# Optimization experiments

Measured on AMD Instinct MI355X. Metric: run time of the kernel, lower is better.

## Reference

```python
import jax, jax.numpy as jnp
import numpy as np

B, N, IN, OUT, H, F = 4, 2048, 128, 64, 4, 64


def setup_inputs() -> dict:
    key = jax.random.key(0)
    ks = jax.random.split(key, 10)
    h = jax.random.normal(ks[0], (B, N, IN), dtype=jnp.float32)
    projection_matrix = jax.random.uniform(ks[1], (B, N, N), dtype=jnp.float32)
    similarity_matrix = jnp.tanh(jax.random.normal(ks[2], (B, N, N), dtype=jnp.float32))
    quadrant_matrix = jax.random.randint(ks[3], (B, N, N, 2), 0, 4)
    # learned params (xavier-ish scaling); stored as (in, out) so x @ W
    W = jax.random.normal(ks[4], (IN, OUT * H), dtype=jnp.float32) * (1.0 / np.sqrt(IN))
    random_projection = jax.random.normal(ks[5], (IN, F), dtype=jnp.float32) * 0.1
    a_q = jax.random.normal(ks[6], (2 * F, OUT), dtype=jnp.float32) * (1.0 / np.sqrt(2 * F))
    a_k = jax.random.normal(ks[7], (2 * F, OUT), dtype=jnp.float32) * (1.0 / np.sqrt(2 * F))
    quadrant_bias = jax.random.normal(ks[8], (4, 4), dtype=jnp.float32) * 0.02
    output_proj = jax.random.normal(ks[9], (OUT * H, OUT), dtype=jnp.float32) * (1.0 / np.sqrt(OUT * H))
    return {
        "h": h,
        "projection_matrix": projection_matrix,
        "similarity_matrix": similarity_matrix,
        "W": W,
        "random_projection": random_projection,
        "a_q": a_q,
        "a_k": a_k,
        "quadrant_bias": quadrant_bias,
        "output_proj": output_proj,
        "quadrant_matrix": quadrant_matrix,
    }


def reference(h, projection_matrix, similarity_matrix, W, random_projection,
              a_q, a_k, quadrant_bias, output_proj, quadrant_matrix):
    # random feature map: phi = [cos(h R), sin(h R)]  -> (B, N, 2F)
    proj = jnp.einsum('bnd,df->bnf', h, random_projection)
    phi = jnp.concatenate([jnp.cos(proj), jnp.sin(proj)], axis=-1)
    Q = phi @ a_q                       # (B, N, OUT)
    K = phi @ a_k                       # (B, N, OUT)
    Wh = (h @ W).reshape(h.shape[0], h.shape[1], H, OUT)  # (B, N, H, OUT)

    scores = jnp.einsum('bio,bjo->bij', Q, K)             # (B, N, N)
    # additive relational biases (shared across heads)
    qb = quadrant_bias[quadrant_matrix[..., 0], quadrant_matrix[..., 1]]  # (B, N, N)
    scores = scores + projection_matrix + similarity_matrix + qb
    attn = jax.nn.softmax(scores[:, None, :, :], axis=-1)  # (B, H, N, N) via broadcast

    # aggregate values per head, then concat heads
    hp = jnp.einsum('bhij,bjhk->bihk', attn, Wh)           # (B, N, H, OUT)
    hp = hp.reshape(h.shape[0], h.shape[1], H * OUT)
    out = hp @ output_proj                                  # (B, N, OUT)
    return jax.nn.elu(out)
```

## Files before the change

### kernel.cpp

```cpp
#include <hip/hip_runtime.h>
#include <math.h>

#define BB   4
#define NN   2048
#define IND  128
#define CDIM 256
#define NIT  16

typedef _Float16 half_t;
typedef _Float16 half4_t __attribute__((ext_vector_type(4)));
typedef _Float16 half8_t __attribute__((ext_vector_type(8)));
typedef float    f32x4   __attribute__((ext_vector_type(4)));

#define SHIFT 16.0f

__global__ __launch_bounds__(256) void precompute_kernel(
    const float* __restrict__ hg,
    const float* __restrict__ W,
    const float* __restrict__ R,
    const float* __restrict__ aq,
    const float* __restrict__ ak,
    half_t* __restrict__ Qw,
    half_t* __restrict__ Kw,
    half_t* __restrict__ WhJ)
{
    const int tid  = threadIdx.x;
    const int row0 = blockIdx.x * 16;

    __shared__ float hs[16][IND];
    __shared__ float phis[16][IND];

    {
        const float4* src = (const float4*)(hg + (size_t)row0 * IND);
        float4* dst = (float4*)&hs[0][0];
        dst[tid]       = src[tid];
        dst[tid + 256] = src[tid + 256];
    }
    __syncthreads();

    {
        const int f  = tid & 63;
        const int rr = tid >> 6;
        float p0 = 0.f, p1 = 0.f, p2 = 0.f, p3 = 0.f;
        #pragma unroll 8
        for (int d = 0; d < IND; ++d) {
            const float rv = R[d * 64 + f];
            p0 += hs[rr][d] * rv;      p1 += hs[rr + 4][d] * rv;
            p2 += hs[rr + 8][d] * rv;  p3 += hs[rr + 12][d] * rv;
        }
        float s, c;
        __sincosf(p0, &s, &c); phis[rr][f]      = c; phis[rr][f + 64]      = s;
        __sincosf(p1, &s, &c); phis[rr + 4][f]  = c; phis[rr + 4][f + 64]  = s;
        __sincosf(p2, &s, &c); phis[rr + 8][f]  = c; phis[rr + 8][f + 64]  = s;
        __sincosf(p3, &s, &c); phis[rr + 12][f] = c; phis[rr + 12][f + 64] = s;
    }

    {
        float acc[16];
        #pragma unroll
        for (int r = 0; r < 16; ++r) acc[r] = 0.f;
        #pragma unroll 4
        for (int d = 0; d < IND; ++d) {
            const float w = W[d * CDIM + tid];
            #pragma unroll
            for (int r = 0; r < 16; ++r) acc[r] += hs[r][d] * w;
        }
        const int b   = row0 >> 11;
        const int j16 = (row0 & (NN - 1)) >> 4;
        half8_t v0, v1;
        #pragma unroll
        for (int r = 0; r < 8; ++r) { v0[r] = (half_t)acc[r]; v1[r] = (half_t)acc[r + 8]; }
        half8_t* dst = (half8_t*)(WhJ + (((size_t)b * 128 + j16) * CDIM + tid) * 16);
        dst[0] = v0; dst[1] = v1;
    }
    __syncthreads();

    {
        const int o  = tid & 63;
        const int qk = (tid >> 6) & 1;
        const int rh = tid >> 7;
        const float* A = qk ? ak : aq;
        half_t*    Dst = qk ? Kw : Qw;
        float acc[8];
        #pragma unroll
        for (int r = 0; r < 8; ++r) acc[r] = 0.f;
        #pragma unroll 4
        for (int tt = 0; tt < IND; ++tt) {
            const float a = A[tt * 64 + o];
            #pragma unroll
            for (int r = 0; r < 8; ++r) acc[r] += phis[rh * 8 + r][tt] * a;
        }
        #pragma unroll
        for (int r = 0; r < 8; ++r)
            Dst[(size_t)(row0 + rh * 8 + r) * 64 + o] = (half_t)acc[r];
    }
}

__global__ __launch_bounds__(512, 4) void attn3_kernel(
    const half_t* __restrict__ Qw, const half_t* __restrict__ Kw,
    const half_t* __restrict__ WhJ,
    const float* __restrict__ pm,
    const float* __restrict__ sm,
    const int*   __restrict__ qm,
    const float* __restrict__ qbias,
    const float* __restrict__ op,
    float* __restrict__ out)
{
    const int tid  = threadIdx.x;
    const int w    = tid >> 6;
    const int lane = tid & 63;
    const int n    = lane & 15;
    const int q    = lane >> 4;

    const int blk = blockIdx.x;
    const int b   = (blk & 7) >> 1;
    const int i0  = (((blk >> 3) << 1) | (blk & 1)) * 16;

    __shared__ __align__(16) float BufT0[CDIM][20];
    __shared__ __align__(16) float BufT1[CDIM][20];
    __shared__ float Lp[8][16];
    __shared__ float qbs[16];

    if (tid < 16) qbs[tid] = qbias[tid] - SHIFT;
    __syncthreads();

    const half_t* qptr = Qw + ((size_t)(b * NN) + i0 + n) * 64;
    const half8_t qf0 = *(const half8_t*)(qptr + q * 8);
    const half8_t qf1 = *(const half8_t*)(qptr + 32 + q * 8);

    const size_t rowoff = ((size_t)b * NN + i0 + n) * NN;
    const float* pmr = pm + rowoff;
    const float* smr = sm + rowoff;
    const int*   qmr = qm + rowoff * 2;
    const int cbase = w * 16 + q * 4;

    float4 pmN = *(const float4*)(pmr + cbase);
    float4 smN = *(const float4*)(smr + cbase);
    int4   qmN0 = *(const int4*)(qmr + cbase * 2);
    int4   qmN1 = *(const int4*)(qmr + cbase * 2 + 4);

    const half_t* kbase = Kw + ((size_t)b * NN + w * 16 + n) * 64;
    const half_t* wbase = WhJ + (((size_t)b * 128 + w) * CDIM + n) * 16 + q * 4;

    f32x4 acc[16];
    #pragma unroll
    for (int t = 0; t < 16; ++t) acc[t] = (f32x4){0.f, 0.f, 0.f, 0.f};
    float lacc = 0.f;

    for (int it = 0; it < NIT; ++it) {
        const half_t* kp = kbase + (size_t)it * 128 * 64;
        const half8_t kf0 = *(const half8_t*)(kp + q * 8);
        const half8_t kf1 = *(const half8_t*)(kp + 32 + q * 8);
        f32x4 s4 = (f32x4){0.f, 0.f, 0.f, 0.f};
        s4 = __builtin_amdgcn_mfma_f32_16x16x32_f16(kf0, qf0, s4, 0, 0, 0);
        s4 = __builtin_amdgcn_mfma_f32_16x16x32_f16(kf1, qf1, s4, 0, 0, 0);

        const float4 pmC = pmN; const float4 smC = smN;
        const int4 qA = qmN0;  const int4 qB = qmN1;
        if (it + 1 < NIT) {
            const int jn = (it + 1) * 128 + cbase;
            pmN  = *(const float4*)(pmr + jn);
            smN  = *(const float4*)(smr + jn);
            qmN0 = *(const int4*)(qmr + jn * 2);
            qmN1 = *(const int4*)(qmr + jn * 2 + 4);
        }

        float sv0 = s4[0] + pmC.x + smC.x + qbs[qA.x * 4 + qA.y];
        float sv1 = s4[1] + pmC.y + smC.y + qbs[qA.z * 4 + qA.w];
        float sv2 = s4[2] + pmC.z + smC.z + qbs[qB.x * 4 + qB.y];
        float sv3 = s4[3] + pmC.w + smC.w + qbs[qB.z * 4 + qB.w];

        half4_t aP;
        const half_t h0 = (half_t)__expf(fminf(sv0, 11.f));
        const half_t h1 = (half_t)__expf(fminf(sv1, 11.f));
        const half_t h2 = (half_t)__expf(fminf(sv2, 11.f));
        const half_t h3 = (half_t)__expf(fminf(sv3, 11.f));
        aP[0] = h0; aP[1] = h1; aP[2] = h2; aP[3] = h3;
        lacc += (float)h0 + (float)h1 + (float)h2 + (float)h3;

        const half_t* wp = wbase + (size_t)it * 8 * CDIM * 16;
        #pragma unroll
        for (int ct = 0; ct < 16; ++ct) {
            const half4_t bW = *(const half4_t*)(wp + (size_t)ct * 16 * 16);
            acc[ct] = __builtin_amdgcn_mfma_f32_16x16x16f16(aP, bW, acc[ct], 0, 0, 0);
        }
    }

    lacc += __shfl_xor(lacc, 16);
    lacc += __shfl_xor(lacc, 32);
    if (lane < 16) Lp[w][lane] = lacc;

    #pragma unroll
    for (int rnd = 0; rnd < 4; ++rnd) {
        __syncthreads();
        if ((w >> 1) == rnd) {
            float* Bf = (w & 1) ? &BufT1[0][0] : &BufT0[0][0];
            #pragma unroll
            for (int ct = 0; ct < 16; ++ct) {
                float* p = Bf + (ct * 16 + n) * 20 + q * 4;
                if (rnd == 0) *(f32x4*)p = acc[ct];
                else          *(f32x4*)p = *(const f32x4*)p + acc[ct];
            }
        }
    }
    __syncthreads();
    {
        f32x4* a = (f32x4*)&BufT0[0][0];
        const f32x4* c = (const f32x4*)&BufT1[0][0];
        for (int idx = tid; idx < CDIM * 5; idx += 512) a[idx] = a[idx] + c[idx];
    }
    __syncthreads();

    {
        const int r0 = 2 * w, r1 = 2 * w + 1;
        float acc0 = 0.f, acc1 = 0.f;
        #pragma unroll 8
        for (int c = 0; c < CDIM; ++c) {
            const float wv = op[c * 64 + lane];
            acc0 += BufT0[c][r0] * wv;
            acc1 += BufT0[c][r1] * wv;
        }
        float lt0 = 0.f, lt1 = 0.f;
        #pragma unroll
        for (int gg = 0; gg < 8; ++gg) { lt0 += Lp[gg][r0]; lt1 += Lp[gg][r1]; }
        float x0 = acc0 / lt0;
        float x1 = acc1 / lt1;
        x0 = x0 > 0.f ? x0 : (__expf(x0) - 1.f);
        x1 = x1 > 0.f ? x1 : (__expf(x1) - 1.f);
        out[((size_t)b * NN + i0 + r0) * 64 + lane] = x0;
        out[((size_t)b * NN + i0 + r1) * 64 + lane] = x1;
    }
}

extern "C" void kernel_launch(void* const* d_in, const int* in_sizes, int n_in,
                              void* d_out, int out_size, void* d_ws, size_t ws_size,
                              hipStream_t stream) {
    (void)in_sizes; (void)n_in; (void)out_size; (void)ws_size;
    const float* h  = (const float*)d_in[0];
    const float* pm = (const float*)d_in[1];
    const float* sm = (const float*)d_in[2];
    const float* W  = (const float*)d_in[3];
    const float* R  = (const float*)d_in[4];
    const float* aq = (const float*)d_in[5];
    const float* ak = (const float*)d_in[6];
    const float* qb = (const float*)d_in[7];
    const float* op = (const float*)d_in[8];
    const int*   qm = (const int*)d_in[9];
    float* out = (float*)d_out;

    half_t* ws  = (half_t*)d_ws;
    half_t* Qw  = ws;
    half_t* Kw  = ws + (size_t)BB * NN * 64;
    half_t* WhJ = ws + (size_t)BB * NN * 64 * 2;

    precompute_kernel<<<BB * NN / 16, 256, 0, stream>>>(h, W, R, aq, ak, Qw, Kw, WhJ);
    attn3_kernel<<<BB * (NN / 16), 512, 0, stream>>>(Qw, Kw, WhJ, pm, sm, qm, qb, op, out);
}
```

Before: 370.8 us.

## Pre-fuse additive biases into packed 16-bit buffer before attention

Adds a streaming kernel that sums the projection, similarity and quadrant-bias terms and quantizes them to 16-bit fixed point in workspace. The attention kernel then reads 2 bytes per score instead of 16, and its loop is unrolled by two with double-buffered K and bias prefetch. The aim is to move the heavy irregular loads out of the MFMA loop, at the cost of an extra full pass over the inputs plus a write and re-read of the packed buffer, and some quantization error. The precompute kernel is also retiled to 8 rows per block with vectorized shared-memory reads. A fallback keeps the old path when the workspace is too small.

```diff
diff --git a/kernel.cpp b/kernel.cpp
--- a/kernel.cpp
+++ b/kernel.cpp
@@ -13,6 +13,37 @@
 typedef float    f32x4   __attribute__((ext_vector_type(4)));
 
 #define SHIFT 16.0f
+#define BSCL  6.103515625e-05f
+#define BOFF  (-17.5f)
+
+__global__ __launch_bounds__(256) void fuse_bias_kernel(
+    const float* __restrict__ pm, const float* __restrict__ sm,
+    const int*   __restrict__ qm, const float* __restrict__ qbias,
+    unsigned short* __restrict__ bf)
+{
+    __shared__ float qbs[16];
+    if (threadIdx.x < 16) qbs[threadIdx.x] = qbias[threadIdx.x];
+    __syncthreads();
+
+    const int nquad  = BB * NN * NN / 4;
+    const int stride = gridDim.x * 256;
+    for (int idx = blockIdx.x * 256 + threadIdx.x; idx < nquad; idx += stride) {
+        const float4 p  = ((const float4*)pm)[idx];
+        const float4 s  = ((const float4*)sm)[idx];
+        const int4   qa = ((const int4*)qm)[(size_t)idx * 2];
+        const int4   qb = ((const int4*)qm)[(size_t)idx * 2 + 1];
+        const float f0 = p.x + s.x + qbs[(qa.x << 2) | qa.y];
+        const float f1 = p.y + s.y + qbs[(qa.z << 2) | qa.w];
+        const float f2 = p.z + s.z + qbs[(qb.x << 2) | qb.y];
+        const float f3 = p.w + s.w + qbs[(qb.z << 2) | qb.w];
+        const unsigned u0 = __float2uint_rn(fminf(fmaxf((f0 + 1.5f) * 16384.f, 0.f), 65535.f));
+        const unsigned u1 = __float2uint_rn(fminf(fmaxf((f1 + 1.5f) * 16384.f, 0.f), 65535.f));
+        const unsigned u2 = __float2uint_rn(fminf(fmaxf((f2 + 1.5f) * 16384.f, 0.f), 65535.f));
+        const unsigned u3 = __float2uint_rn(fminf(fmaxf((f3 + 1.5f) * 16384.f, 0.f), 65535.f));
+        uint2 o; o.x = u0 | (u1 << 16); o.y = u2 | (u3 << 16);
+        ((uint2*)bf)[idx] = o;
+    }
+}
 
 __global__ __launch_bounds__(256) void precompute_kernel(
     const float* __restrict__ hg,
@@ -25,53 +56,60 @@
     half_t* __restrict__ WhJ)
 {
     const int tid  = threadIdx.x;
-    const int row0 = blockIdx.x * 16;
-
-    __shared__ float hs[16][IND];
-    __shared__ float phis[16][IND];
+    const int row0 = blockIdx.x * 8;
+
+    __shared__ float hs[8][IND];
+    __shared__ float phis[8][IND];
 
     {
         const float4* src = (const float4*)(hg + (size_t)row0 * IND);
-        float4* dst = (float4*)&hs[0][0];
-        dst[tid]       = src[tid];
-        dst[tid + 256] = src[tid + 256];
+        ((float4*)&hs[0][0])[tid] = src[tid];
     }
     __syncthreads();
 
     {
         const int f  = tid & 63;
         const int rr = tid >> 6;
-        float p0 = 0.f, p1 = 0.f, p2 = 0.f, p3 = 0.f;
-        #pragma unroll 8
-        for (int d = 0; d < IND; ++d) {
-            const float rv = R[d * 64 + f];
-            p0 += hs[rr][d] * rv;      p1 += hs[rr + 4][d] * rv;
-            p2 += hs[rr + 8][d] * rv;  p3 += hs[rr + 12][d] * rv;
+        float p0 = 0.f, p1 = 0.f;
+        #pragma unroll 4
+        for (int d0 = 0; d0 < IND; d0 += 4) {
+            const float r0 = R[(d0 + 0) * 64 + f];
+            const float r1 = R[(d0 + 1) * 64 + f];
+            const float r2 = R[(d0 + 2) * 64 + f];
+            const float r3 = R[(d0 + 3) * 64 + f];
+            const float4 ha = *(const float4*)&hs[rr][d0];
+            const float4 hb = *(const float4*)&hs[rr + 4][d0];
+            p0 += ha.x * r0 + ha.y * r1 + ha.z * r2 + ha.w * r3;
+            p1 += hb.x * r0 + hb.y * r1 + hb.z * r2 + hb.w * r3;
         }
         float s, c;
-        __sincosf(p0, &s, &c); phis[rr][f]      = c; phis[rr][f + 64]      = s;
-        __sincosf(p1, &s, &c); phis[rr + 4][f]  = c; phis[rr + 4][f + 64]  = s;
-        __sincosf(p2, &s, &c); phis[rr + 8][f]  = c; phis[rr + 8][f + 64]  = s;
-        __sincosf(p3, &s, &c); phis[rr + 12][f] = c; phis[rr + 12][f + 64] = s;
-    }
-
-    {
-        float acc[16];
-        #pragma unroll
-        for (int r = 0; r < 16; ++r) acc[r] = 0.f;
-        #pragma unroll 4
-        for (int d = 0; d < IND; ++d) {
-            const float w = W[d * CDIM + tid];
+        __sincosf(p0, &s, &c); phis[rr][f]     = c; phis[rr][f + 64]     = s;
+        __sincosf(p1, &s, &c); phis[rr + 4][f] = c; phis[rr + 4][f + 64] = s;
+    }
+
+    {
+        float acc[8];
+        #pragma unroll
+        for (int r = 0; r < 8; ++r) acc[r] = 0.f;
+        #pragma unroll 2
+        for (int d0 = 0; d0 < IND; d0 += 4) {
+            const float w0 = W[(d0 + 0) * CDIM + tid];
+            const float w1 = W[(d0 + 1) * CDIM + tid];
+            const float w2 = W[(d0 + 2) * CDIM + tid];
+            const float w3 = W[(d0 + 3) * CDIM + tid];
             #pragma unroll
-            for (int r = 0; r < 16; ++r) acc[r] += hs[r][d] * w;
+            for (int r = 0; r < 8; ++r) {
+                const float4 h4 = *(const float4*)&hs[r][d0];
+                acc[r] += h4.x * w0 + h4.y * w1 + h4.z * w2 + h4.w * w3;
+            }
         }
         const int b   = row0 >> 11;
         const int j16 = (row0 & (NN - 1)) >> 4;
-        half8_t v0, v1;
-        #pragma unroll
-        for (int r = 0; r < 8; ++r) { v0[r] = (half_t)acc[r]; v1[r] = (half_t)acc[r + 8]; }
-        half8_t* dst = (half8_t*)(WhJ + (((size_t)b * 128 + j16) * CDIM + tid) * 16);
-        dst[0] = v0; dst[1] = v1;
+        const int jr0 = row0 & 8;
+        half8_t v;
+        #pragma unroll
+        for (int r = 0; r < 8; ++r) v[r] = (half_t)acc[r];
+        *(half8_t*)(WhJ + (((size_t)b * 128 + j16) * CDIM + tid) * 16 + jr0) = v;
     }
     __syncthreads();
 
@@ -81,28 +119,60 @@
         const int rh = tid >> 7;
         const float* A = qk ? ak : aq;
         half_t*    Dst = qk ? Kw : Qw;
-        float acc[8];
-        #pragma unroll
-        for (int r = 0; r < 8; ++r) acc[r] = 0.f;
-        #pragma unroll 4
-        for (int tt = 0; tt < IND; ++tt) {
-            const float a = A[tt * 64 + o];
+        float acc[4] = {0.f, 0.f, 0.f, 0.f};
+        #pragma unroll 2
+        for (int t0 = 0; t0 < IND; t0 += 4) {
+            const float a0 = A[(t0 + 0) * 64 + o];
+            const float a1 = A[(t0 + 1) * 64 + o];
+            const float a2 = A[(t0 + 2) * 64 + o];
+            const float a3 = A[(t0 + 3) * 64 + o];
             #pragma unroll
-            for (int r = 0; r < 8; ++r) acc[r] += phis[rh * 8 + r][tt] * a;
-        }
-        #pragma unroll
-        for (int r = 0; r < 8; ++r)
-            Dst[(size_t)(row0 + rh * 8 + r) * 64 + o] = (half_t)acc[r];
+            for (int r = 0; r < 4; ++r) {
+                const float4 ph = *(const float4*)&phis[rh * 4 + r][t0];
+                acc[r] += ph.x * a0 + ph.y * a1 + ph.z * a2 + ph.w * a3;
+            }
+        }
+        #pragma unroll
+        for (int r = 0; r < 4; ++r)
+            Dst[(size_t)(row0 + rh * 4 + r) * 64 + o] = (half_t)acc[r];
     }
 }
+
+#define ITER(IT, UB, KC0, KC1, KN0, KN1)                                       \
+  {                                                                            \
+    f32x4 s4 = (f32x4){0.f, 0.f, 0.f, 0.f};                                    \
+    s4 = __builtin_amdgcn_mfma_f32_16x16x32_f16(KC0, qf0, s4, 0, 0, 0);        \
+    s4 = __builtin_amdgcn_mfma_f32_16x16x32_f16(KC1, qf1, s4, 0, 0, 0);        \
+    if ((IT) + 1 < NIT) {                                                      \
+      const half_t* kp = kbase + (size_t)((IT) + 1) * 128 * 64;                \
+      KN0 = *(const half8_t*)(kp + q * 8);                                     \
+      KN1 = *(const half8_t*)(kp + 32 + q * 8);                                \
+    }                                                                          \
+    const uint2 uc = UB;                                                       \
+    if ((IT) + 2 < NIT)                                                        \
+      UB = *(const uint2*)(bfr + (size_t)((IT) + 2) * 128 + cbase);            \
+    const float b0 = fmaf((float)(uc.x & 0xffffu), BSCL, BOFF);                \
+    const float b1 = fmaf((float)(uc.x >> 16),     BSCL, BOFF);                \
+    const float b2 = fmaf((float)(uc.y & 0xffffu), BSCL, BOFF);                \
+    const float b3 = fmaf((float)(uc.y >> 16),     BSCL, BOFF);                \
+    const half_t h0 = (half_t)__expf(fminf(s4[0] + b0, 11.f));                 \
+    const half_t h1 = (half_t)__expf(fminf(s4[1] + b1, 11.f));                 \
+    const half_t h2 = (half_t)__expf(fminf(s4[2] + b2, 11.f));                 \
+    const half_t h3 = (half_t)__expf(fminf(s4[3] + b3, 11.f));                 \
+    half4_t aP; aP[0] = h0; aP[1] = h1; aP[2] = h2; aP[3] = h3;                \
+    lacc += (float)h0 + (float)h1 + (float)h2 + (float)h3;                     \
+    const half_t* wp = wbase + (size_t)(IT) * 8 * CDIM * 16;                   \
+    _Pragma("unroll")                                                          \
+    for (int ct = 0; ct < 16; ++ct) {                                          \
+      const half4_t bW = *(const half4_t*)(wp + (size_t)ct * 256);             \
+      acc[ct] = __builtin_amdgcn_mfma_f32_16x16x16f16(aP, bW, acc[ct], 0, 0, 0);\
+    }                                                                          \
+  }
 
 __global__ __launch_bounds__(512, 4) void attn3_kernel(
     const half_t* __restrict__ Qw, const half_t* __restrict__ Kw,
     const half_t* __restrict__ WhJ,
-    const float* __restrict__ pm,
-    const float* __restrict__ sm,
-    const int*   __restrict__ qm,
-    const float* __restrict__ qbias,
+    const unsigned short* __restrict__ bf,
     const float* __restrict__ op,
     float* __restrict__ out)
 {
@@ -119,71 +189,32 @@
     __shared__ __align__(16) float BufT0[CDIM][20];
     __shared__ __align__(16) float BufT1[CDIM][20];
     __shared__ float Lp[8][16];
-    __shared__ float qbs[16];
-
-    if (tid < 16) qbs[tid] = qbias[tid] - SHIFT;
-    __syncthreads();
 
     const half_t* qptr = Qw + ((size_t)(b * NN) + i0 + n) * 64;
     const half8_t qf0 = *(const half8_t*)(qptr + q * 8);
     const half8_t qf1 = *(const half8_t*)(qptr + 32 + q * 8);
 
     const size_t rowoff = ((size_t)b * NN + i0 + n) * NN;
-    const float* pmr = pm + rowoff;
-    const float* smr = sm + rowoff;
-    const int*   qmr = qm + rowoff * 2;
+    const unsigned short* bfr = bf + rowoff;
     const int cbase = w * 16 + q * 4;
-
-    float4 pmN = *(const float4*)(pmr + cbase);
-    float4 smN = *(const float4*)(smr + cbase);
-    int4   qmN0 = *(const int4*)(qmr + cbase * 2);
-    int4   qmN1 = *(const int4*)(qmr + cbase * 2 + 4);
 
     const half_t* kbase = Kw + ((size_t)b * NN + w * 16 + n) * 64;
     const half_t* wbase = WhJ + (((size_t)b * 128 + w) * CDIM + n) * 16 + q * 4;
+
+    uint2 ub0 = *(const uint2*)(bfr + cbase);
+    uint2 ub1 = *(const uint2*)(bfr + 128 + cbase);
+    half8_t ka0 = *(const half8_t*)(kbase + q * 8);
+    half8_t ka1 = *(const half8_t*)(kbase + 32 + q * 8);
+    half8_t kb0 = ka0, kb1 = ka1;
 
     f32x4 acc[16];
     #pragma unroll
     for (int t = 0; t < 16; ++t) acc[t] = (f32x4){0.f, 0.f, 0.f, 0.f};
     float lacc = 0.f;
 
-    for (int it = 0; it < NIT; ++it) {
-        const half_t* kp = kbase + (size_t)it * 128 * 64;
-        const half8_t kf0 = *(const half8_t*)(kp + q * 8);
-        const half8_t kf1 = *(const half8_t*)(kp + 32 + q * 8);
-        f32x4 s4 = (f32x4){0.f, 0.f, 0.f, 0.f};
-        s4 = __builtin_amdgcn_mfma_f32_16x16x32_f16(kf0, qf0, s4, 0, 0, 0);
-        s4 = __builtin_amdgcn_mfma_f32_16x16x32_f16(kf1, qf1, s4, 0, 0, 0);
-
-        const float4 pmC = pmN; const float4 smC = smN;
-        const int4 qA = qmN0;  const int4 qB = qmN1;
-        if (it + 1 < NIT) {
-            const int jn = (it + 1) * 128 + cbase;
-            pmN  = *(const float4*)(pmr + jn);
-            smN  = *(const float4*)(smr + jn);
-            qmN0 = *(const int4*)(qmr + jn * 2);
-            qmN1 = *(const int4*)(qmr + jn * 2 + 4);
-        }
-
-        float sv0 = s4[0] + pmC.x + smC.x + qbs[qA.x * 4 + qA.y];
-        float sv1 = s4[1] + pmC.y + smC.y + qbs[qA.z * 4 + qA.w];
-        float sv2 = s4[2] + pmC.z + smC.z + qbs[qB.x * 4 + qB.y];
-        float sv3 = s4[3] + pmC.w + smC.w + qbs[qB.z * 4 + qB.w];
-
-        half4_t aP;
-        const half_t h0 = (half_t)__expf(fminf(sv0, 11.f));
-        const half_t h1 = (half_t)__expf(fminf(sv1, 11.f));
-        const half_t h2 = (half_t)__expf(fminf(sv2, 11.f));
-        const half_t h3 = (half_t)__expf(fminf(sv3, 11.f));
-        aP[0] = h0; aP[1] = h1; aP[2] = h2; aP[3] = h3;
-        lacc += (float)h0 + (float)h1 + (float)h2 + (float)h3;
-
-        const half_t* wp = wbase + (size_t)it * 8 * CDIM * 16;
-        #pragma unroll
-        for (int ct = 0; ct < 16; ++ct) {
-            const half4_t bW = *(const half4_t*)(wp + (size_t)ct * 16 * 16);
-            acc[ct] = __builtin_amdgcn_mfma_f32_16x16x16f16(aP, bW, acc[ct], 0, 0, 0);
-        }
+    for (int it = 0; it < NIT; it += 2) {
+        ITER(it,     ub0, ka0, ka1, kb0, kb1)
+        ITER(it + 1, ub1, kb0, kb1, ka0, ka1)
     }
 
     lacc += __shfl_xor(lacc, 16);
@@ -232,10 +263,143 @@
     }
 }
 
+__global__ __launch_bounds__(512, 4) void attn3_fb_kernel(
+    const half_t* __restrict__ Qw, const half_t* __restrict__ Kw,
+    const half_t* __restrict__ WhJ,
+    const float* __restrict__ pm, const float* __restrict__ sm,
+    const int*   __restrict__ qm, const float* __restrict__ qbias,
+    const float* __restrict__ op, float* __restrict__ out)
+{
+    const int tid  = threadIdx.x;
+    const int w    = tid >> 6;
+    const int lane = tid & 63;
+    const int n    = lane & 15;
+    const int q    = lane >> 4;
+
+    const int blk = blockIdx.x;
+    const int b   = (blk & 7) >> 1;
+    const int i0  = (((blk >> 3) << 1) | (blk & 1)) * 16;
+
+    __shared__ __align__(16) float BufT0[CDIM][20];
+    __shared__ __align__(16) float BufT1[CDIM][20];
+    __shared__ float Lp[8][16];
+    __shared__ float qbs[16];
+
+    if (tid < 16) qbs[tid] = qbias[tid] - SHIFT;
+    __syncthreads();
+
+    const half_t* qptr = Qw + ((size_t)(b * NN) + i0 + n) * 64;
+    const half8_t qf0 = *(const half8_t*)(qptr + q * 8);
+    const half8_t qf1 = *(const half8_t*)(qptr + 32 + q * 8);
+
+    const size_t rowoff = ((size_t)b * NN + i0 + n) * NN;
+    const float* pmr = pm + rowoff;
+    const float* smr = sm + rowoff;
+    const int*   qmr = qm + rowoff * 2;
+    const int cbase = w * 16 + q * 4;
+
+    float4 pmN = *(const float4*)(pmr + cbase);
+    float4 smN = *(const float4*)(smr + cbase);
+    int4   qmN0 = *(const int4*)(qmr + cbase * 2);
+    int4   qmN1 = *(const int4*)(qmr + cbase * 2 + 4);
+
+    const half_t* kbase = Kw + ((size_t)b * NN + w * 16 + n) * 64;
+    const half_t* wbase = WhJ + (((size_t)b * 128 + w) * CDIM + n) * 16 + q * 4;
+
+    f32x4 acc[16];
+    #pragma unroll
+    for (int t = 0; t < 16; ++t) acc[t] = (f32x4){0.f, 0.f, 0.f, 0.f};
+    float lacc = 0.f;
+
+    for (int it = 0; it < NIT; ++it) {
+        const half_t* kp = kbase + (size_t)it * 128 * 64;
+        const half8_t kf0 = *(const half8_t*)(kp + q * 8);
+        const half8_t kf1 = *(const half8_t*)(kp + 32 + q * 8);
+        f32x4 s4 = (f32x4){0.f, 0.f, 0.f, 0.f};
+        s4 = __builtin_amdgcn_mfma_f32_16x16x32_f16(kf0, qf0, s4, 0, 0, 0);
+        s4 = __builtin_amdgcn_mfma_f32_16x16x32_f16(kf1, qf1, s4, 0, 0, 0);
+
+        const float4 pmC = pmN; const float4 smC = smN;
+        const int4 qA = qmN0;  const int4 qB = qmN1;
+        if (it + 1 < NIT) {
+            const int jn = (it + 1) * 128 + cbase;
+            pmN  = *(const float4*)(pmr + jn);
+            smN  = *(const float4*)(smr + jn);
+            qmN0 = *(const int4*)(qmr + jn * 2);
+            qmN1 = *(const int4*)(qmr + jn * 2 + 4);
+        }
+
+        float sv0 = s4[0] + pmC.x + smC.x + qbs[qA.x * 4 + qA.y];
+        float sv1 = s4[1] + pmC.y + smC.y + qbs[qA.z * 4 + qA.w];
+        float sv2 = s4[2] + pmC.z + smC.z + qbs[qB.x * 4 + qB.y];
+        float sv3 = s4[3] + pmC.w + smC.w + qbs[qB.z * 4 + qB.w];
+
+        half4_t aP;
+        const half_t h0 = (half_t)__expf(fminf(sv0, 11.f));
+        const half_t h1 = (half_t)__expf(fminf(sv1, 11.f));
+        const half_t h2 = (half_t)__expf(fminf(sv2, 11.f));
+        const half_t h3 = (half_t)__expf(fminf(sv3, 11.f));
+        aP[0] = h0; aP[1] = h1; aP[2] = h2; aP[3] = h3;
+        lacc += (float)h0 + (float)h1 + (float)h2 + (float)h3;
+
+        const half_t* wp = wbase + (size_t)it * 8 * CDIM * 16;
+        #pragma unroll
+        for (int ct = 0; ct < 16; ++ct) {
+            const half4_t bW = *(const half4_t*)(wp + (size_t)ct * 16 * 16);
+            acc[ct] = __builtin_amdgcn_mfma_f32_16x16x16f16(aP, bW, acc[ct], 0, 0, 0);
+        }
+    }
+
+    lacc += __shfl_xor(lacc, 16);
+    lacc += __shfl_xor(lacc, 32);
+    if (lane < 16) Lp[w][lane] = lacc;
+
+    #pragma unroll
+    for (int rnd = 0; rnd < 4; ++rnd) {
+        __syncthreads();
+        if ((w >> 1) == rnd) {
+            float* Bf = (w & 1) ? &BufT1[0][0] : &BufT0[0][0];
+            #pragma unroll
+            for (int ct = 0; ct < 16; ++ct) {
+                float* p = Bf + (ct * 16 + n) * 20 + q * 4;
+                if (rnd == 0) *(f32x4*)p = acc[ct];
+                else          *(f32x4*)p = *(const f32x4*)p + acc[ct];
+            }
+        }
+    }
+    __syncthreads();
+    {
+        f32x4* a = (f32x4*)&BufT0[0][0];
+        const f32x4* c = (const f32x4*)&BufT1[0][0];
+        for (int idx = tid; idx < CDIM * 5; idx += 512) a[idx] = a[idx] + c[idx];
+    }
+    __syncthreads();
+
+    {
+        const int r0 = 2 * w, r1 = 2 * w + 1;
+        float acc0 = 0.f, acc1 = 0.f;
+        #pragma unroll 8
+        for (int c = 0; c < CDIM; ++c) {
+            const float wv = op[c * 64 + lane];
+            acc0 += BufT0[c][r0] * wv;
+            acc1 += BufT0[c][r1] * wv;
+        }
+        float lt0 = 0.f, lt1 = 0.f;
+        #pragma unroll
+        for (int gg = 0; gg < 8; ++gg) { lt0 += Lp[gg][r0]; lt1 += Lp[gg][r1]; }
+        float x0 = acc0 / lt0;
+        float x1 = acc1 / lt1;
+        x0 = x0 > 0.f ? x0 : (__expf(x0) - 1.f);
+        x1 = x1 > 0.f ? x1 : (__expf(x1) - 1.f);
+        out[((size_t)b * NN + i0 + r0) * 64 + lane] = x0;
+        out[((size_t)b * NN + i0 + r1) * 64 + lane] = x1;
+    }
+}
+
 extern "C" void kernel_launch(void* const* d_in, const int* in_sizes, int n_in,
                               void* d_out, int out_size, void* d_ws, size_t ws_size,
                               hipStream_t stream) {
-    (void)in_sizes; (void)n_in; (void)out_size; (void)ws_size;
+    (void)in_sizes; (void)n_in; (void)out_size;
     const float* h  = (const float*)d_in[0];
     const float* pm = (const float*)d_in[1];
     const float* sm = (const float*)d_in[2];
@@ -252,7 +416,17 @@
     half_t* Qw  = ws;
     half_t* Kw  = ws + (size_t)BB * NN * 64;
     half_t* WhJ = ws + (size_t)BB * NN * 64 * 2;
-
-    precompute_kernel<<<BB * NN / 16, 256, 0, stream>>>(h, W, R, aq, ak, Qw, Kw, WhJ);
-    attn3_kernel<<<BB * (NN / 16), 512, 0, stream>>>(Qw, Kw, WhJ, pm, sm, qm, qb, op, out);
+    unsigned short* bf =
+        (unsigned short*)(ws + (size_t)BB * NN * 64 * 2 + (size_t)BB * NN * CDIM);
+
+    const size_t need = ((size_t)BB * NN * 64 * 2 + (size_t)BB * NN * CDIM) * sizeof(half_t)
+                      + (size_t)BB * NN * NN * sizeof(unsigned short);
+
+    precompute_kernel<<<BB * NN / 8, 256, 0, stream>>>(h, W, R, aq, ak, Qw, Kw, WhJ);
+    if (ws_size >= need) {
+        fuse_bias_kernel<<<2048, 256, 0, stream>>>(pm, sm, qm, qb, bf);
+        attn3_kernel<<<BB * (NN / 16), 512, 0, stream>>>(Qw, Kw, WhJ, bf, op, out);
+    } else {
+        attn3_fb_kernel<<<BB * (NN / 16), 512, 0, stream>>>(Qw, Kw, WhJ, pm, sm, qm, qb, op, out);
+    }
 }
```

New measurement: 427.3 us. +15.2%, slower.

## Repartition attention value matmul across waves via LDS-shared probabilities

Applied to the files above, without the earlier changes.

The attention kernel now has each wave own 32 output channels instead of all 256. Each wave writes its exp-probability fragment into double-buffered LDS, and after a barrier every wave reads all eight key fragments and does the value MFMAs for its own channel slice. This drops the 16-accumulator-per-wave layout and the four-round cross-wave reduction through two LDS buffers, at the cost of one barrier per key tile. Value loads are issued early and K fragments are register double-buffered via a macro-unrolled loop. Separately, the precompute kernel handles 8 rows per block with float4 LDS reads, doubling its grid.

```diff
diff --git a/kernel.cpp b/kernel.cpp
--- a/kernel.cpp
+++ b/kernel.cpp
@@ -25,53 +25,60 @@
     half_t* __restrict__ WhJ)
 {
     const int tid  = threadIdx.x;
-    const int row0 = blockIdx.x * 16;
-
-    __shared__ float hs[16][IND];
-    __shared__ float phis[16][IND];
+    const int row0 = blockIdx.x * 8;
+
+    __shared__ float hs[8][IND];
+    __shared__ float phis[8][IND];
 
     {
         const float4* src = (const float4*)(hg + (size_t)row0 * IND);
-        float4* dst = (float4*)&hs[0][0];
-        dst[tid]       = src[tid];
-        dst[tid + 256] = src[tid + 256];
+        ((float4*)&hs[0][0])[tid] = src[tid];
     }
     __syncthreads();
 
     {
         const int f  = tid & 63;
         const int rr = tid >> 6;
-        float p0 = 0.f, p1 = 0.f, p2 = 0.f, p3 = 0.f;
-        #pragma unroll 8
-        for (int d = 0; d < IND; ++d) {
-            const float rv = R[d * 64 + f];
-            p0 += hs[rr][d] * rv;      p1 += hs[rr + 4][d] * rv;
-            p2 += hs[rr + 8][d] * rv;  p3 += hs[rr + 12][d] * rv;
+        float p0 = 0.f, p1 = 0.f;
+        #pragma unroll 4
+        for (int d0 = 0; d0 < IND; d0 += 4) {
+            const float r0 = R[(d0 + 0) * 64 + f];
+            const float r1 = R[(d0 + 1) * 64 + f];
+            const float r2 = R[(d0 + 2) * 64 + f];
+            const float r3 = R[(d0 + 3) * 64 + f];
+            const float4 ha = *(const float4*)&hs[rr][d0];
+            const float4 hb = *(const float4*)&hs[rr + 4][d0];
+            p0 += ha.x * r0 + ha.y * r1 + ha.z * r2 + ha.w * r3;
+            p1 += hb.x * r0 + hb.y * r1 + hb.z * r2 + hb.w * r3;
         }
         float s, c;
-        __sincosf(p0, &s, &c); phis[rr][f]      = c; phis[rr][f + 64]      = s;
-        __sincosf(p1, &s, &c); phis[rr + 4][f]  = c; phis[rr + 4][f + 64]  = s;
-        __sincosf(p2, &s, &c); phis[rr + 8][f]  = c; phis[rr + 8][f + 64]  = s;
-        __sincosf(p3, &s, &c); phis[rr + 12][f] = c; phis[rr + 12][f + 64] = s;
-    }
-
-    {
-        float acc[16];
-        #pragma unroll
-        for (int r = 0; r < 16; ++r) acc[r] = 0.f;
-        #pragma unroll 4
-        for (int d = 0; d < IND; ++d) {
-            const float w = W[d * CDIM + tid];
+        __sincosf(p0, &s, &c); phis[rr][f]     = c; phis[rr][f + 64]     = s;
+        __sincosf(p1, &s, &c); phis[rr + 4][f] = c; phis[rr + 4][f + 64] = s;
+    }
+
+    {
+        float acc[8];
+        #pragma unroll
+        for (int r = 0; r < 8; ++r) acc[r] = 0.f;
+        #pragma unroll 2
+        for (int d0 = 0; d0 < IND; d0 += 4) {
+            const float w0 = W[(d0 + 0) * CDIM + tid];
+            const float w1 = W[(d0 + 1) * CDIM + tid];
+            const float w2 = W[(d0 + 2) * CDIM + tid];
+            const float w3 = W[(d0 + 3) * CDIM + tid];
             #pragma unroll
-            for (int r = 0; r < 16; ++r) acc[r] += hs[r][d] * w;
+            for (int r = 0; r < 8; ++r) {
+                const float4 h4 = *(const float4*)&hs[r][d0];
+                acc[r] += h4.x * w0 + h4.y * w1 + h4.z * w2 + h4.w * w3;
+            }
         }
         const int b   = row0 >> 11;
         const int j16 = (row0 & (NN - 1)) >> 4;
-        half8_t v0, v1;
-        #pragma unroll
-        for (int r = 0; r < 8; ++r) { v0[r] = (half_t)acc[r]; v1[r] = (half_t)acc[r + 8]; }
-        half8_t* dst = (half8_t*)(WhJ + (((size_t)b * 128 + j16) * CDIM + tid) * 16);
-        dst[0] = v0; dst[1] = v1;
+        const int jr0 = row0 & 8;
+        half8_t v;
+        #pragma unroll
+        for (int r = 0; r < 8; ++r) v[r] = (half_t)acc[r];
+        *(half8_t*)(WhJ + (((size_t)b * 128 + j16) * CDIM + tid) * 16 + jr0) = v;
     }
     __syncthreads();
 
@@ -81,22 +88,77 @@
         const int rh = tid >> 7;
         const float* A = qk ? ak : aq;
         half_t*    Dst = qk ? Kw : Qw;
-        float acc[8];
-        #pragma unroll
-        for (int r = 0; r < 8; ++r) acc[r] = 0.f;
-        #pragma unroll 4
-        for (int tt = 0; tt < IND; ++tt) {
-            const float a = A[tt * 64 + o];
+        float acc[4] = {0.f, 0.f, 0.f, 0.f};
+        #pragma unroll 2
+        for (int t0 = 0; t0 < IND; t0 += 4) {
+            const float a0 = A[(t0 + 0) * 64 + o];
+            const float a1 = A[(t0 + 1) * 64 + o];
+            const float a2 = A[(t0 + 2) * 64 + o];
+            const float a3 = A[(t0 + 3) * 64 + o];
             #pragma unroll
-            for (int r = 0; r < 8; ++r) acc[r] += phis[rh * 8 + r][tt] * a;
-        }
-        #pragma unroll
-        for (int r = 0; r < 8; ++r)
-            Dst[(size_t)(row0 + rh * 8 + r) * 64 + o] = (half_t)acc[r];
+            for (int r = 0; r < 4; ++r) {
+                const float4 ph = *(const float4*)&phis[rh * 4 + r][t0];
+                acc[r] += ph.x * a0 + ph.y * a1 + ph.z * a2 + ph.w * a3;
+            }
+        }
+        #pragma unroll
+        for (int r = 0; r < 4; ++r)
+            Dst[(size_t)(row0 + rh * 4 + r) * 64 + o] = (half_t)acc[r];
     }
 }
 
-__global__ __launch_bounds__(512, 4) void attn3_kernel(
+#define ITER(IT, KC0, KC1, KN0, KN1, PB)                                        \
+  {                                                                             \
+       \
+    const half_t* wpt = wb + (size_t)(IT) * (8 * CDIM * 16);                    \
+    half4_t bwv[16];                                                            \
+    _Pragma("unroll")                                                           \
+    for (int kk = 0; kk < 8; ++kk) {                                            \
+      bwv[2 * kk]     = *(const half4_t*)(wpt + (size_t)kk * (CDIM * 16));      \
+      bwv[2 * kk + 1] = *(const half4_t*)(wpt + (size_t)kk * (CDIM * 16) + 256);\
+    }                                                                           \
+                                     \
+    f32x4 s4 = (f32x4){0.f, 0.f, 0.f, 0.f};                                     \
+    s4 = __builtin_amdgcn_mfma_f32_16x16x32_f16(KC0, qf0, s4, 0, 0, 0);         \
+    s4 = __builtin_amdgcn_mfma_f32_16x16x32_f16(KC1, qf1, s4, 0, 0, 0);         \
+    if ((IT) + 1 < NIT) {                                                       \
+      const half_t* kp = kbase + (size_t)((IT) + 1) * 128 * 64;                 \
+      KN0 = *(const half8_t*)(kp + q * 8);                                      \
+      KN1 = *(const half8_t*)(kp + 32 + q * 8);                                 \
+    }                                                                           \
+    const float4 pmC = pmN; const float4 smC = smN;                             \
+    const int4 qA = qmN0;  const int4 qB = qmN1;                                \
+    if ((IT) + 1 < NIT) {                                                       \
+      const int jn = ((IT) + 1) * 128 + cbase;                                  \
+      pmN  = *(const float4*)(pmr + jn);                                        \
+      smN  = *(const float4*)(smr + jn);                                        \
+      qmN0 = *(const int4*)(qmr + (size_t)jn * 2);                              \
+      qmN1 = *(const int4*)(qmr + (size_t)jn * 2 + 4);                          \
+    }                                                                           \
+    const float sv0 = s4[0] + pmC.x + smC.x + qbs[qA.x * 4 + qA.y];             \
+    const float sv1 = s4[1] + pmC.y + smC.y + qbs[qA.z * 4 + qA.w];             \
+    const float sv2 = s4[2] + pmC.z + smC.z + qbs[qB.x * 4 + qB.y];             \
+    const float sv3 = s4[3] + pmC.w + smC.w + qbs[qB.z * 4 + qB.w];             \
+    const half_t h0 = (half_t)__expf(fminf(sv0, 11.f));                         \
+    const half_t h1 = (half_t)__expf(fminf(sv1, 11.f));                         \
+    const half_t h2 = (half_t)__expf(fminf(sv2, 11.f));                         \
+    const half_t h3 = (half_t)__expf(fminf(sv3, 11.f));                         \
+    half4_t aP; aP[0] = h0; aP[1] = h1; aP[2] = h2; aP[3] = h3;                 \
+    lacc += (float)h0 + (float)h1 + (float)h2 + (float)h3;                      \
+    *(half4_t*)&Pl[PB][w][lane * 4] = aP;                                       \
+    asm volatile("s_waitcnt lgkmcnt(0)" ::: "memory");                          \
+    __builtin_amdgcn_s_barrier();                                               \
+    asm volatile("" ::: "memory");                                              \
+                 \
+    _Pragma("unroll")                                                           \
+    for (int kk = 0; kk < 8; ++kk) {                                            \
+      const half4_t pa = *(const half4_t*)&Pl[PB][kk][lane * 4];                \
+      acc0 = __builtin_amdgcn_mfma_f32_16x16x16f16(pa, bwv[2 * kk],     acc0, 0, 0, 0); \
+      acc1 = __builtin_amdgcn_mfma_f32_16x16x16f16(pa, bwv[2 * kk + 1], acc1, 0, 0, 0); \
+    }                                                                           \
+  }
+
+__global__ __launch_bounds__(512, 4) void attn4_kernel(
     const half_t* __restrict__ Qw, const half_t* __restrict__ Kw,
     const half_t* __restrict__ WhJ,
     const float* __restrict__ pm,
@@ -116,8 +178,8 @@
     const int b   = (blk & 7) >> 1;
     const int i0  = (((blk >> 3) << 1) | (blk & 1)) * 16;
 
-    __shared__ __align__(16) float BufT0[CDIM][20];
-    __shared__ __align__(16) float BufT1[CDIM][20];
+    __shared__ __align__(16) half_t Pl[2][8][256];
+    __shared__ __align__(16) float  BufT0[CDIM][20];
     __shared__ float Lp[8][16];
     __shared__ float qbs[16];
 
@@ -134,97 +196,48 @@
     const int*   qmr = qm + rowoff * 2;
     const int cbase = w * 16 + q * 4;
 
-    float4 pmN = *(const float4*)(pmr + cbase);
-    float4 smN = *(const float4*)(smr + cbase);
+    const half_t* kbase = Kw + ((size_t)b * NN + w * 16 + n) * 64;
+    const half_t* wb = WhJ + ((size_t)b * 128 * CDIM + (size_t)(w * 32 + n)) * 16 + q * 4;
+
+    float4 pmN  = *(const float4*)(pmr + cbase);
+    float4 smN  = *(const float4*)(smr + cbase);
     int4   qmN0 = *(const int4*)(qmr + cbase * 2);
     int4   qmN1 = *(const int4*)(qmr + cbase * 2 + 4);
-
-    const half_t* kbase = Kw + ((size_t)b * NN + w * 16 + n) * 64;
-    const half_t* wbase = WhJ + (((size_t)b * 128 + w) * CDIM + n) * 16 + q * 4;
-
-    f32x4 acc[16];
-    #pragma unroll
-    for (int t = 0; t < 16; ++t) acc[t] = (f32x4){0.f, 0.f, 0.f, 0.f};
+    half8_t ka0 = *(const half8_t*)(kbase + q * 8);
+    half8_t ka1 = *(const half8_t*)(kbase + 32 + q * 8);
+    half8_t kb0 = ka0, kb1 = ka1;
+
+    f32x4 acc0 = (f32x4){0.f, 0.f, 0.f, 0.f};
+    f32x4 acc1 = (f32x4){0.f, 0.f, 0.f, 0.f};
     float lacc = 0.f;
 
-    for (int it = 0; it < NIT; ++it) {
-        const half_t* kp = kbase + (size_t)it * 128 * 64;
-        const half8_t kf0 = *(const half8_t*)(kp + q * 8);
-        const half8_t kf1 = *(const half8_t*)(kp + 32 + q * 8);
-        f32x4 s4 = (f32x4){0.f, 0.f, 0.f, 0.f};
-        s4 = __builtin_amdgcn_mfma_f32_16x16x32_f16(kf0, qf0, s4, 0, 0, 0);
-        s4 = __builtin_amdgcn_mfma_f32_16x16x32_f16(kf1, qf1, s4, 0, 0, 0);
-
-        const float4 pmC = pmN; const float4 smC = smN;
-        const int4 qA = qmN0;  const int4 qB = qmN1;
-        if (it + 1 < NIT) {
-            const int jn = (it + 1) * 128 + cbase;
-            pmN  = *(const float4*)(pmr + jn);
-            smN  = *(const float4*)(smr + jn);
-            qmN0 = *(const int4*)(qmr + jn * 2);
-            qmN1 = *(const int4*)(qmr + jn * 2 + 4);
-        }
-
-        float sv0 = s4[0] + pmC.x + smC.x + qbs[qA.x * 4 + qA.y];
-        float sv1 = s4[1] + pmC.y + smC.y + qbs[qA.z * 4 + qA.w];
-        float sv2 = s4[2] + pmC.z + smC.z + qbs[qB.x * 4 + qB.y];
-        float sv3 = s4[3] + pmC.w + smC.w + qbs[qB.z * 4 + qB.w];
-
-        half4_t aP;
-        const half_t h0 = (half_t)__expf(fminf(sv0, 11.f));
-        const half_t h1 = (half_t)__expf(fminf(sv1, 11.f));
-        const half_t h2 = (half_t)__expf(fminf(sv2, 11.f));
-        const half_t h3 = (half_t)__expf(fminf(sv3, 11.f));
-        aP[0] = h0; aP[1] = h1; aP[2] = h2; aP[3] = h3;
-        lacc += (float)h0 + (float)h1 + (float)h2 + (float)h3;
-
-        const half_t* wp = wbase + (size_t)it * 8 * CDIM * 16;
-        #pragma unroll
-        for (int ct = 0; ct < 16; ++ct) {
-            const half4_t bW = *(const half4_t*)(wp + (size_t)ct * 16 * 16);
-            acc[ct] = __builtin_amdgcn_mfma_f32_16x16x16f16(aP, bW, acc[ct], 0, 0, 0);
-        }
+    for (int it = 0; it < NIT; it += 2) {
+        ITER(it,     ka0, ka1, kb0, kb1, 0)
+        ITER(it + 1, kb0, kb1, ka0, ka1, 1)
     }
 
     lacc += __shfl_xor(lacc, 16);
     lacc += __shfl_xor(lacc, 32);
     if (lane < 16) Lp[w][lane] = lacc;
 
-    #pragma unroll
-    for (int rnd = 0; rnd < 4; ++rnd) {
-        __syncthreads();
-        if ((w >> 1) == rnd) {
-            float* Bf = (w & 1) ? &BufT1[0][0] : &BufT0[0][0];
-            #pragma unroll
-            for (int ct = 0; ct < 16; ++ct) {
-                float* p = Bf + (ct * 16 + n) * 20 + q * 4;
-                if (rnd == 0) *(f32x4*)p = acc[ct];
-                else          *(f32x4*)p = *(const f32x4*)p + acc[ct];
-            }
-        }
-    }
-    __syncthreads();
-    {
-        f32x4* a = (f32x4*)&BufT0[0][0];
-        const f32x4* c = (const f32x4*)&BufT1[0][0];
-        for (int idx = tid; idx < CDIM * 5; idx += 512) a[idx] = a[idx] + c[idx];
-    }
+    *(f32x4*)&BufT0[w * 32 + n][q * 4]      = acc0;
+    *(f32x4*)&BufT0[w * 32 + 16 + n][q * 4] = acc1;
     __syncthreads();
 
     {
         const int r0 = 2 * w, r1 = 2 * w + 1;
-        float acc0 = 0.f, acc1 = 0.f;
+        float pacc0 = 0.f, pacc1 = 0.f;
         #pragma unroll 8
         for (int c = 0; c < CDIM; ++c) {
             const float wv = op[c * 64 + lane];
-            acc0 += BufT0[c][r0] * wv;
-            acc1 += BufT0[c][r1] * wv;
+            pacc0 += BufT0[c][r0] * wv;
+            pacc1 += BufT0[c][r1] * wv;
         }
         float lt0 = 0.f, lt1 = 0.f;
         #pragma unroll
         for (int gg = 0; gg < 8; ++gg) { lt0 += Lp[gg][r0]; lt1 += Lp[gg][r1]; }
-        float x0 = acc0 / lt0;
-        float x1 = acc1 / lt1;
+        float x0 = pacc0 / lt0;
+        float x1 = pacc1 / lt1;
         x0 = x0 > 0.f ? x0 : (__expf(x0) - 1.f);
         x1 = x1 > 0.f ? x1 : (__expf(x1) - 1.f);
         out[((size_t)b * NN + i0 + r0) * 64 + lane] = x0;
@@ -253,6 +266,6 @@
     half_t* Kw  = ws + (size_t)BB * NN * 64;
     half_t* WhJ = ws + (size_t)BB * NN * 64 * 2;
 
-    precompute_kernel<<<BB * NN / 16, 256, 0, stream>>>(h, W, R, aq, ak, Qw, Kw, WhJ);
-    attn3_kernel<<<BB * (NN / 16), 512, 0, stream>>>(Qw, Kw, WhJ, pm, sm, qm, qb, op, out);
+    precompute_kernel<<<BB * NN / 8, 256, 0, stream>>>(h, W, R, aq, ak, Qw, Kw, WhJ);
+    attn4_kernel<<<BB * (NN / 16), 512, 0, stream>>>(Qw, Kw, WhJ, pm, sm, qm, qb, op, out);
 }
```

Result: faster. 349.7 us (-5.7%).
